# Kernel optimization log

Measured on AMD Instinct MI355X. Metric: run time of the kernel, lower is better.

Reference implementation:

```python
import jax, jax.numpy as jnp
import numpy as np

B, D_IN, D_OUT, E = 8192, 1024, 1024, 16


def setup_inputs() -> dict:
    key = jax.random.key(0)
    k1, k2, k3 = jax.random.split(key, 3)
    x = jax.random.normal(k1, (B, D_IN), dtype=jnp.float32)
    Wg = jax.random.normal(k2, (D_IN, E), dtype=jnp.float32) * (1.0 / np.sqrt(D_IN))
    bg = jnp.zeros((E,), dtype=jnp.float32)
    We = jax.random.normal(k3, (E, D_IN, D_OUT), dtype=jnp.float32) * (1.0 / np.sqrt(D_IN))
    be = jnp.zeros((E, D_OUT), dtype=jnp.float32)
    return {"x": x, "Wg": Wg, "bg": bg, "We": We, "be": be}


def reference(x, Wg, bg, We, be):
    # Gate: [B, E]
    gate_out = x @ Wg + bg
    top1 = jnp.argmax(gate_out, axis=1)  # [B]
    # All-expert dense compute (faithful to the naive HardMoE): [B, E, D_OUT]
    expert_outs = jnp.einsum('bd,edh->beh', x, We) + be[None, :, :]
    # Gather each row's argmax expert output: [B, D_OUT]
    out = jnp.take_along_axis(expert_outs, top1[:, None, None], axis=1)[:, 0, :]
    return out
```

## Files before the change

kernel.cpp:

```cpp
#include <hip/hip_runtime.h>

typedef unsigned short u16;
typedef __attribute__((ext_vector_type(4))) unsigned short u16x4;
typedef __attribute__((ext_vector_type(8))) short short8;
typedef __attribute__((ext_vector_type(4))) float floatx4;

#define NB 8192
#define DK 1024
#define DN 1024
#define NE 16
#define TM 128
#define TN 128
#define BK 64
#define MAX_TILES 80

#define GATE_BLOCKS 256
#define WET_BLOCKS  4096

__device__ __forceinline__ u16 f2bf(float f) {
    union { float f; unsigned int u; } v; v.f = f;
    unsigned int u = v.u;
    return (u16)((u + 0x7fffu + ((u >> 16) & 1u)) >> 16);
}

__device__ __forceinline__ void gld16(const void* g, void* l) {
    __builtin_amdgcn_global_load_lds(
        (const __attribute__((address_space(1))) unsigned int*)g,
        (__attribute__((address_space(3))) unsigned int*)l, 16, 0, 0);
}

__global__ __launch_bounds__(256) void k_prep(const float* __restrict__ x,
                                              const float* __restrict__ Wg,
                                              const float* __restrict__ bg,
                                              const float* __restrict__ We,
                                              u16* __restrict__ xb,
                                              u16* __restrict__ WeT,
                                              int* __restrict__ cnt,
                                              int* __restrict__ bucket) {
    __shared__ union {
        struct { float xs[32 * 132]; float wgs[16 * 132]; } g;
        u16 t[64 * 68];
    } sh;

    const int tid = threadIdx.x;

    if (blockIdx.x < GATE_BLOCKS) {
        const int kg = tid & 7;
        const int eg = (tid >> 3) & 3;
        const int rg = tid >> 5;
        const int R0 = blockIdx.x * 32;

        float* xs  = sh.g.xs;
        float* wgs = sh.g.wgs;

        double acc[4][4];
        #pragma unroll
        for (int i = 0; i < 4; ++i)
            #pragma unroll
            for (int j = 0; j < 4; ++j) acc[i][j] = 0.0;

        for (int c = 0; c < 8; ++c) {
            const int k0 = c * 128;
            #pragma unroll
            for (int it = 0; it < 4; ++it) {
                int f = it * 256 + tid;
                int r = f >> 5;
                int k4 = (f & 31) * 4;
                float4 v = *(const float4*)&x[(size_t)(R0 + r) * DK + k0 + k4];
                *(float4*)&xs[r * 132 + k4] = v;
                u16x4 b; b.x = f2bf(v.x); b.y = f2bf(v.y); b.z = f2bf(v.z); b.w = f2bf(v.w);
                *(u16x4*)&xb[(size_t)(R0 + r) * DK + k0 + k4] = b;
            }
            #pragma unroll
            for (int it = 0; it < 2; ++it) {
                int g = it * 256 + tid;
                int k = g >> 2;
                int e4 = (g & 3) * 4;
                float4 v = *(const float4*)&Wg[(size_t)(k0 + k) * NE + e4];
                wgs[(e4 + 0) * 132 + k] = v.x;
                wgs[(e4 + 1) * 132 + k] = v.y;
                wgs[(e4 + 2) * 132 + k] = v.z;
                wgs[(e4 + 3) * 132 + k] = v.w;
            }
            __syncthreads();
            #pragma unroll
            for (int t = 0; t < 4; ++t) {
                const int ko = t * 32 + kg * 4;
                float4 xq[4], wq[4];
                #pragma unroll
                for (int i = 0; i < 4; ++i)
                    xq[i] = *(const float4*)&xs[(rg * 4 + i) * 132 + ko];
                #pragma unroll
                for (int j = 0; j < 4; ++j)
                    wq[j] = *(const float4*)&wgs[(eg * 4 + j) * 132 + ko];
                #pragma unroll
                for (int i = 0; i < 4; ++i)
                    #pragma unroll
                    for (int j = 0; j < 4; ++j) {
                        acc[i][j] += (double)xq[i].x * (double)wq[j].x;
                        acc[i][j] += (double)xq[i].y * (double)wq[j].y;
                        acc[i][j] += (double)xq[i].z * (double)wq[j].z;
                        acc[i][j] += (double)xq[i].w * (double)wq[j].w;
                    }
            }
            __syncthreads();
        }

        #pragma unroll
        for (int i = 0; i < 4; ++i)
            #pragma unroll
            for (int j = 0; j < 4; ++j) {
                double v = acc[i][j];
                v += __shfl_xor(v, 1);
                v += __shfl_xor(v, 2);
                v += __shfl_xor(v, 4);
                acc[i][j] = v + (double)bg[eg * 4 + j];
            }

        #pragma unroll
        for (int i = 0; i < 4; ++i) {
            double best = acc[i][0]; int bi = eg * 4;
            #pragma unroll
            for (int j = 1; j < 4; ++j)
                if (acc[i][j] > best) { best = acc[i][j]; bi = eg * 4 + j; }
            #pragma unroll
            for (int off = 8; off <= 16; off <<= 1) {
                double ov = __shfl_xor(best, off);
                int    oi = __shfl_xor(bi, off);
                if (ov > best || (ov == best && oi < bi)) { best = ov; bi = oi; }
            }
            if (kg == 0 && eg == 0) {
                int pos = atomicAdd(&cnt[bi], 1);
                bucket[bi * NB + pos] = R0 + rg * 4 + i;
            }
        }
    } else {
        const int bw = blockIdx.x - GATE_BLOCKS;
        const int e  = bw >> 8;
        const int n0 = ((bw >> 4) & 15) * 64;
        const int k0 = (bw & 15) * 64;
        u16* t = sh.t;
        const float* src = We + (size_t)e * DK * DN;
        const int kl = tid >> 4;
        const int n4 = (tid & 15) * 4;
        #pragma unroll
        for (int r = 0; r < 4; ++r) {
            int k = kl + r * 16;
            float4 v = *(const float4*)&src[(size_t)(k0 + k) * DN + n0 + n4];
            t[(n4 + 0) * 68 + k] = f2bf(v.x);
            t[(n4 + 1) * 68 + k] = f2bf(v.y);
            t[(n4 + 2) * 68 + k] = f2bf(v.z);
            t[(n4 + 3) * 68 + k] = f2bf(v.w);
        }
        __syncthreads();
        u16* dst = WeT + (size_t)e * DN * DK;
        #pragma unroll
        for (int r = 0; r < 4; ++r) {
            int c = r * 256 + tid;
            int nl = c >> 4;
            int kq = (c & 15) * 4;
            *(u16x4*)&dst[(size_t)(n0 + nl) * DK + k0 + kq] = *(const u16x4*)&t[nl * 68 + kq];
        }
    }
}

__global__ __launch_bounds__(256) void k_moe(const u16* __restrict__ xb,
                                             const u16* __restrict__ WeT,
                                             const float* __restrict__ be,
                                             const int* __restrict__ bucket,
                                             const int* __restrict__ cnt,
                                             float* __restrict__ out) {
    const int slot = blockIdx.x >> 3;
    const int nt = blockIdx.x & 7;

    int e = -1, mt = 0, cntE = 0, acc_t = 0;
    #pragma unroll
    for (int ee = 0; ee < NE; ++ee) {
        int ce = cnt[ee];
        int nte = (ce + TM - 1) / TM;
        if (e < 0 && slot < acc_t + nte) { e = ee; mt = slot - acc_t; cntE = ce; }
        acc_t += nte;
    }
    if (e < 0) return;

    const int m0 = mt * TM;
    const int n0 = nt * TN;

    __shared__ u16 aLds[TM * BK];
    __shared__ u16 bLds[TN * BK];

    const int tid = threadIdx.x;
    const int lane = tid & 63;
    const int w = tid >> 6;
    const int wr = w >> 1, wc = w & 1;
    const int lr = lane & 15, q = lane >> 4;

    long aoff[4]; long boff[4]; int ldsb[4];
    #pragma unroll
    for (int r = 0; r < 4; ++r) {
        int c = r * 256 + tid;
        int row = c >> 3;
        int k8 = (c & 7) ^ (row & 7);
        int m_idx = m0 + row; if (m_idx >= cntE) m_idx = cntE - 1;
        long rid = bucket[e * NB + m_idx];
        aoff[r] = rid * DK + k8 * 8;
        boff[r] = (long)e * DN * DK + (long)(n0 + row) * DK + k8 * 8;
        ldsb[r] = (r * 256 + (tid & ~63)) * 8;
    }

    floatx4 acc[4][4];
    #pragma unroll
    for (int mi = 0; mi < 4; ++mi)
        #pragma unroll
        for (int ni = 0; ni < 4; ++ni)
            acc[mi][ni] = (floatx4)0.0f;

    for (int kk = 0; kk < DK; kk += BK) {
        #pragma unroll
        for (int r = 0; r < 4; ++r) {
            gld16(xb + aoff[r] + kk, &aLds[ldsb[r]]);
            gld16(WeT + boff[r] + kk, &bLds[ldsb[r]]);
        }
        __syncthreads();
        #pragma unroll
        for (int ks = 0; ks < 2; ++ks) {
            short8 af[4], bfr[4];
            const int slot_k = ((ks << 2) + q) ^ (lr & 7);
            #pragma unroll
            for (int mi = 0; mi < 4; ++mi) {
                int row = wr * 64 + mi * 16 + lr;
                af[mi] = *(const short8*)&aLds[row * BK + slot_k * 8];
                int nrow = wc * 64 + mi * 16 + lr;
                bfr[mi] = *(const short8*)&bLds[nrow * BK + slot_k * 8];
            }
            #pragma unroll
            for (int mi = 0; mi < 4; ++mi)
                #pragma unroll
                for (int ni = 0; ni < 4; ++ni)
                    acc[mi][ni] = __builtin_amdgcn_mfma_f32_16x16x32_bf16(
                        af[mi], bfr[ni], acc[mi][ni], 0, 0, 0);
        }
        __syncthreads();
    }

    float bias[4];
    #pragma unroll
    for (int ni = 0; ni < 4; ++ni)
        bias[ni] = be[e * DN + n0 + wc * 64 + ni * 16 + lr];

    #pragma unroll
    for (int mi = 0; mi < 4; ++mi) {
        #pragma unroll
        for (int rr = 0; rr < 4; ++rr) {
            int row_l = wr * 64 + mi * 16 + q * 4 + rr;
            int m_idx = m0 + row_l;
            if (m_idx < cntE) {
                long rid = bucket[e * NB + m_idx];
                float* orow = out + rid * DN + n0 + wc * 64 + lr;
                #pragma unroll
                for (int ni = 0; ni < 4; ++ni)
                    orow[ni * 16] = acc[mi][ni][rr] + bias[ni];
            }
        }
    }
}

extern "C" void kernel_launch(void* const* d_in, const int* in_sizes, int n_in,
                              void* d_out, int out_size, void* d_ws, size_t ws_size,
                              hipStream_t stream) {
    const float* x  = (const float*)d_in[0];
    const float* Wg = (const float*)d_in[1];
    const float* bg = (const float*)d_in[2];
    const float* We = (const float*)d_in[3];
    const float* be = (const float*)d_in[4];
    float* out = (float*)d_out;

    int* cnt    = (int*)d_ws;
    int* bucket = cnt + 128;
    u16* xb  = (u16*)((char*)d_ws + (1u << 20));
    u16* wet = (u16*)((char*)d_ws + (18u << 20));

    hipMemsetAsync(cnt, 0, 16 * sizeof(int), stream);
    k_prep<<<GATE_BLOCKS + WET_BLOCKS, 256, 0, stream>>>(x, Wg, bg, We, xb, wet, cnt, bucket);
    k_moe<<<MAX_TILES * 8, 256, 0, stream>>>(xb, wet, be, bucket, cnt, out);
}
```

Baseline: 239.4 us.

## Split prep kernel into separate gate and weight-transpose kernels with finer parallelism

Splits the fused prep kernel into a gate kernel and a weight-transpose kernel. The gate kernel now gives each wave one row instead of a block handling 32 rows, spreading the fp64 gate dot products over 2048 blocks. The transpose keeps the tile in fp32 in padded LDS, converts to bf16 on the way out, and writes 16-byte vectors. This trades one extra kernel launch and the loss of gate/transpose overlap for more parallelism and wider stores. The gate kernel reloads the Wg tile in every block.

```diff
diff --git a/kernel.cpp b/kernel.cpp
--- a/kernel.cpp
+++ b/kernel.cpp
@@ -14,9 +14,6 @@
 #define BK 64
 #define MAX_TILES 80
 
-#define GATE_BLOCKS 256
-#define WET_BLOCKS  4096
-
 __device__ __forceinline__ u16 f2bf(float f) {
     union { float f; unsigned int u; } v; v.f = f;
     unsigned int u = v.u;
@@ -29,138 +26,112 @@
         (__attribute__((address_space(3))) unsigned int*)l, 16, 0, 0);
 }
 
-__global__ __launch_bounds__(256) void k_prep(const float* __restrict__ x,
+__global__ __launch_bounds__(256) void k_gate(const float* __restrict__ x,
                                               const float* __restrict__ Wg,
                                               const float* __restrict__ bg,
-                                              const float* __restrict__ We,
                                               u16* __restrict__ xb,
-                                              u16* __restrict__ WeT,
                                               int* __restrict__ cnt,
                                               int* __restrict__ bucket) {
-    __shared__ union {
-        struct { float xs[32 * 132]; float wgs[16 * 132]; } g;
-        u16 t[64 * 68];
-    } sh;
-
+    __shared__ float xs[4 * 260];
+    __shared__ float wgs[256 * 20];
     const int tid = threadIdx.x;
-
-    if (blockIdx.x < GATE_BLOCKS) {
-        const int kg = tid & 7;
-        const int eg = (tid >> 3) & 3;
-        const int rg = tid >> 5;
-        const int R0 = blockIdx.x * 32;
-
-        float* xs  = sh.g.xs;
-        float* wgs = sh.g.wgs;
-
-        double acc[4][4];
-        #pragma unroll
-        for (int i = 0; i < 4; ++i)
-            #pragma unroll
-            for (int j = 0; j < 4; ++j) acc[i][j] = 0.0;
-
-        for (int c = 0; c < 8; ++c) {
-            const int k0 = c * 128;
-            #pragma unroll
-            for (int it = 0; it < 4; ++it) {
-                int f = it * 256 + tid;
-                int r = f >> 5;
-                int k4 = (f & 31) * 4;
-                float4 v = *(const float4*)&x[(size_t)(R0 + r) * DK + k0 + k4];
-                *(float4*)&xs[r * 132 + k4] = v;
-                u16x4 b; b.x = f2bf(v.x); b.y = f2bf(v.y); b.z = f2bf(v.z); b.w = f2bf(v.w);
-                *(u16x4*)&xb[(size_t)(R0 + r) * DK + k0 + k4] = b;
-            }
-            #pragma unroll
-            for (int it = 0; it < 2; ++it) {
-                int g = it * 256 + tid;
-                int k = g >> 2;
-                int e4 = (g & 3) * 4;
-                float4 v = *(const float4*)&Wg[(size_t)(k0 + k) * NE + e4];
-                wgs[(e4 + 0) * 132 + k] = v.x;
-                wgs[(e4 + 1) * 132 + k] = v.y;
-                wgs[(e4 + 2) * 132 + k] = v.z;
-                wgs[(e4 + 3) * 132 + k] = v.w;
-            }
-            __syncthreads();
-            #pragma unroll
-            for (int t = 0; t < 4; ++t) {
-                const int ko = t * 32 + kg * 4;
-                float4 xq[4], wq[4];
-                #pragma unroll
-                for (int i = 0; i < 4; ++i)
-                    xq[i] = *(const float4*)&xs[(rg * 4 + i) * 132 + ko];
-                #pragma unroll
-                for (int j = 0; j < 4; ++j)
-                    wq[j] = *(const float4*)&wgs[(eg * 4 + j) * 132 + ko];
-                #pragma unroll
-                for (int i = 0; i < 4; ++i)
-                    #pragma unroll
-                    for (int j = 0; j < 4; ++j) {
-                        acc[i][j] += (double)xq[i].x * (double)wq[j].x;
-                        acc[i][j] += (double)xq[i].y * (double)wq[j].y;
-                        acc[i][j] += (double)xq[i].z * (double)wq[j].z;
-                        acc[i][j] += (double)xq[i].w * (double)wq[j].w;
-                    }
-            }
-            __syncthreads();
-        }
-
-        #pragma unroll
-        for (int i = 0; i < 4; ++i)
-            #pragma unroll
-            for (int j = 0; j < 4; ++j) {
-                double v = acc[i][j];
-                v += __shfl_xor(v, 1);
-                v += __shfl_xor(v, 2);
-                v += __shfl_xor(v, 4);
-                acc[i][j] = v + (double)bg[eg * 4 + j];
-            }
-
-        #pragma unroll
-        for (int i = 0; i < 4; ++i) {
-            double best = acc[i][0]; int bi = eg * 4;
-            #pragma unroll
-            for (int j = 1; j < 4; ++j)
-                if (acc[i][j] > best) { best = acc[i][j]; bi = eg * 4 + j; }
-            #pragma unroll
-            for (int off = 8; off <= 16; off <<= 1) {
-                double ov = __shfl_xor(best, off);
-                int    oi = __shfl_xor(bi, off);
-                if (ov > best || (ov == best && oi < bi)) { best = ov; bi = oi; }
-            }
-            if (kg == 0 && eg == 0) {
-                int pos = atomicAdd(&cnt[bi], 1);
-                bucket[bi * NB + pos] = R0 + rg * 4 + i;
-            }
-        }
-    } else {
-        const int bw = blockIdx.x - GATE_BLOCKS;
-        const int e  = bw >> 8;
-        const int n0 = ((bw >> 4) & 15) * 64;
-        const int k0 = (bw & 15) * 64;
-        u16* t = sh.t;
-        const float* src = We + (size_t)e * DK * DN;
-        const int kl = tid >> 4;
-        const int n4 = (tid & 15) * 4;
-        #pragma unroll
-        for (int r = 0; r < 4; ++r) {
-            int k = kl + r * 16;
-            float4 v = *(const float4*)&src[(size_t)(k0 + k) * DN + n0 + n4];
-            t[(n4 + 0) * 68 + k] = f2bf(v.x);
-            t[(n4 + 1) * 68 + k] = f2bf(v.y);
-            t[(n4 + 2) * 68 + k] = f2bf(v.z);
-            t[(n4 + 3) * 68 + k] = f2bf(v.w);
-        }
-        __syncthreads();
-        u16* dst = WeT + (size_t)e * DN * DK;
-        #pragma unroll
-        for (int r = 0; r < 4; ++r) {
-            int c = r * 256 + tid;
-            int nl = c >> 4;
-            int kq = (c & 15) * 4;
-            *(u16x4*)&dst[(size_t)(n0 + nl) * DK + k0 + kq] = *(const u16x4*)&t[nl * 68 + kq];
-        }
+    const int lane = tid & 63;
+    const int rg = tid >> 6;
+    const int eg = lane >> 4;
+    const int kg = lane & 15;
+    const int row = blockIdx.x * 4 + rg;
+
+    double acc[4] = {0.0, 0.0, 0.0, 0.0};
+
+    for (int c = 0; c < 4; ++c) {
+        const int k0 = c * 256;
+        {
+            int k4 = (tid & 63) * 4;
+            float4 v = *(const float4*)&x[(size_t)row * DK + k0 + k4];
+            *(float4*)&xs[rg * 260 + k4] = v;
+            u16x4 b; b.x = f2bf(v.x); b.y = f2bf(v.y); b.z = f2bf(v.z); b.w = f2bf(v.w);
+            *(u16x4*)&xb[(size_t)row * DK + k0 + k4] = b;
+        }
+        const float4* Wg4 = (const float4*)Wg + (size_t)c * 1024;
+        #pragma unroll
+        for (int it = 0; it < 4; ++it) {
+            int idx = it * 256 + tid;
+            float4 v = Wg4[idx];
+            *(float4*)&wgs[(idx >> 2) * 20 + (idx & 3) * 4] = v;
+        }
+        __syncthreads();
+        #pragma unroll
+        for (int u = 0; u < 16; ++u) {
+            int k = kg + u * 16;
+            double xv = (double)xs[rg * 260 + k];
+            float4 wq = *(const float4*)&wgs[k * 20 + eg * 4];
+            acc[0] += xv * (double)wq.x;
+            acc[1] += xv * (double)wq.y;
+            acc[2] += xv * (double)wq.z;
+            acc[3] += xv * (double)wq.w;
+        }
+        __syncthreads();
+    }
+
+    #pragma unroll
+    for (int j = 0; j < 4; ++j) {
+        double v = acc[j];
+        v += __shfl_xor(v, 1);
+        v += __shfl_xor(v, 2);
+        v += __shfl_xor(v, 4);
+        v += __shfl_xor(v, 8);
+        acc[j] = v + (double)bg[eg * 4 + j];
+    }
+
+    double best = acc[0]; int bi = eg * 4;
+    #pragma unroll
+    for (int j = 1; j < 4; ++j)
+        if (acc[j] > best) { best = acc[j]; bi = eg * 4 + j; }
+    #pragma unroll
+    for (int off = 16; off <= 32; off <<= 1) {
+        double ov = __shfl_xor(best, off);
+        int    oi = __shfl_xor(bi, off);
+        if (ov > best || (ov == best && oi < bi)) { best = ov; bi = oi; }
+    }
+    if (lane == 0) {
+        int pos = atomicAdd(&cnt[bi], 1);
+        bucket[bi * NB + pos] = row;
+    }
+}
+
+__global__ __launch_bounds__(256) void k_wet(const float* __restrict__ We,
+                                             u16* __restrict__ WeT) {
+    __shared__ float t[64 * 65];
+    const int bw = blockIdx.x;
+    const int e  = bw >> 8;
+    const int n0 = ((bw >> 4) & 15) * 64;
+    const int k0 = (bw & 15) * 64;
+    const int tid = threadIdx.x;
+    const float* src = We + (size_t)e * DK * DN;
+
+    const int n4 = (tid & 15) * 4;
+    const int kl = tid >> 4;
+    #pragma unroll
+    for (int r = 0; r < 4; ++r) {
+        int k = r * 16 + kl;
+        float4 v = *(const float4*)&src[(size_t)(k0 + k) * DN + n0 + n4];
+        t[k * 65 + n4 + 0] = v.x;
+        t[k * 65 + n4 + 1] = v.y;
+        t[k * 65 + n4 + 2] = v.z;
+        t[k * 65 + n4 + 3] = v.w;
+    }
+    __syncthreads();
+    u16* dst = WeT + (size_t)e * DN * DK;
+    #pragma unroll
+    for (int r = 0; r < 2; ++r) {
+        int idx = r * 256 + tid;
+        int nl = idx >> 3;
+        int k8 = idx & 7;
+        u16 pk[8];
+        #pragma unroll
+        for (int i = 0; i < 8; ++i)
+            pk[i] = f2bf(t[(k8 * 8 + i) * 65 + nl]);
+        *(short8*)&dst[(size_t)(n0 + nl) * DK + k0 + k8 * 8] = *(short8*)pk;
     }
 }
 
@@ -281,6 +252,7 @@
     u16* wet = (u16*)((char*)d_ws + (18u << 20));
 
     hipMemsetAsync(cnt, 0, 16 * sizeof(int), stream);
-    k_prep<<<GATE_BLOCKS + WET_BLOCKS, 256, 0, stream>>>(x, Wg, bg, We, xb, wet, cnt, bucket);
+    k_gate<<<2048, 256, 0, stream>>>(x, Wg, bg, xb, cnt, bucket);
+    k_wet<<<4096, 256, 0, stream>>>(We, wet);
     k_moe<<<MAX_TILES * 8, 256, 0, stream>>>(xb, wet, be, bucket, cnt, out);
 }
```

Measured after the change: 284.9 us. 19.0% more time.
